# Optimization experiments

Measured on AMD Instinct MI355X. Metric: run time of the kernel, lower is better.

## Reference

```python
import jax, jax.numpy as jnp
import numpy as np

B = 1_000_000          # query points
D = 3                  # n_input_dims
N_LEVELS = 16
MIN_RES, MAX_RES = 16, 512
N_ENC = 2 ** 19        # max hashmap entries per level
N_EMBED = 2
INIT_SCALE = 1e-4
PRIMES = (1, 2654435761, 805459861)  # instant-ngp spatial-hash primes


def _resolutions():
    # Eq. 2/3 of instant-ngp: geometric growth from MIN_RES to MAX_RES
    growth = np.exp((np.log(MAX_RES) - np.log(MIN_RES)) / (N_LEVELS - 1))
    return [int(np.floor(MIN_RES * growth ** l)) for l in range(N_LEVELS)]

RES = _resolutions()
LEVEL_N_ENC = [min(r ** D, N_ENC) for r in RES]
LEVEL_HASH = [r ** D > N_ENC for r in RES]          # hash iff grid overflows table
CORNERS = np.stack(np.meshgrid(*([np.arange(2)] * D), indexing='ij'), -1).reshape(-1, D)  # (8,3)


def setup_inputs() -> dict:
    key = jax.random.key(0)
    ks = jax.random.split(key, N_LEVELS + 1)
    inp = {"x": jax.random.uniform(ks[0], (B, D), minval=-1.0, maxval=1.0, dtype=jnp.float32)}
    for l in range(N_LEVELS):
        inp[f"emb{l}"] = jax.random.uniform(
            ks[l + 1], (LEVEL_N_ENC[l], N_EMBED), minval=-INIT_SCALE, maxval=INIT_SCALE, dtype=jnp.float32
        )
    return inp


def _level_features(x, emb, res, n_enc, use_hash):
    # x: (B,3) in [-1,1] -> pixel coords, align_corners=False convention
    xp = (x + 1.0) * (res * 0.5) - 0.5
    x0 = jnp.floor(xp)
    t = xp - x0                                           # (B,3) fractional part
    ci = jnp.asarray(CORNERS, jnp.int32)                  # (8,3) corner offsets
    c = x0.astype(jnp.int32)[:, None, :] + ci[None]       # (B,8,3) corner coords
    off = jnp.asarray(CORNERS, xp.dtype)
    # trilinear weights: prod over dims of t or (1-t)
    w = jnp.prod(jnp.where(off[None] > 0, t[:, None, :], 1.0 - t[:, None, :]), axis=-1)  # (B,8)
    m = jnp.all((c >= 0) & (c < res), axis=-1)            # (B,8) zeros-padding mask
    if use_hash:
        cu = c.astype(jnp.uint32)
        h = cu[..., 0] * jnp.uint32(PRIMES[0])
        for d in range(1, D):
            h = h ^ (cu[..., d] * jnp.uint32(PRIMES[d]))
        ids = (h % jnp.uint32(n_enc)).astype(jnp.int32)
    else:
        # ravel index, x varies fastest ('xy' grid indexing)
        ids = (c[..., 0] + c[..., 1] * res + c[..., 2] * res * res) % n_enc
    ids = jnp.where(m, ids, 0)
    w = jnp.where(m, w, jnp.zeros_like(w))
    return jnp.sum(emb[ids] * w[..., None], axis=1)       # (B,E)


def reference(x, emb0, emb1, emb2, emb3, emb4, emb5, emb6, emb7,
              emb8, emb9, emb10, emb11, emb12, emb13, emb14, emb15):
    embs = [emb0, emb1, emb2, emb3, emb4, emb5, emb6, emb7,
            emb8, emb9, emb10, emb11, emb12, emb13, emb14, emb15]
    feats = [_level_features(x, embs[l], RES[l], LEVEL_N_ENC[l], LEVEL_HASH[l])
             for l in range(N_LEVELS)]
    return jnp.stack(feats, axis=1)  # (B, L, E)
```

## Files before the change

### kernel.cpp

```cpp
#include <hip/hip_runtime.h>
#include <stdint.h>


struct EmbPtrs { const float2* p[16]; };

constexpr int BLOCK = 256;
constexpr int kRes[16] = {16,20,25,32,40,50,64,80,101,128,161,203,256,322,406,512};

template<int RES_, bool HASH_>
__device__ __forceinline__ float2 level_feat(const float2* __restrict__ tab,
                                             float px, float py, float pz)
{
    constexpr uint32_t P1 = 2654435761u, P2 = 805459861u;
    constexpr uint32_t HMASK = (1u << 19) - 1u;

    const float rh = (float)RES_ * 0.5f;
    const float xp = (px + 1.0f) * rh - 0.5f;
    const float yp = (py + 1.0f) * rh - 0.5f;
    const float zp = (pz + 1.0f) * rh - 0.5f;
    const float fx = floorf(xp), fy = floorf(yp), fz = floorf(zp);
    const int ix = (int)fx, iy = (int)fy, iz = (int)fz;
    const float tx = xp - fx, ty = yp - fy, tz = zp - fz;

    const float wx[2] = {1.0f - tx, tx};
    const float wy[2] = {1.0f - ty, ty};
    const float wz[2] = {1.0f - tz, tz};
    const bool vx[2] = {(ix   >= 0) && (ix   < RES_), (ix+1 >= 0) && (ix+1 < RES_)};
    const bool vy[2] = {(iy   >= 0) && (iy   < RES_), (iy+1 >= 0) && (iy+1 < RES_)};
    const bool vz[2] = {(iz   >= 0) && (iz   < RES_), (iz+1 >= 0) && (iz+1 < RES_)};

    float ax = 0.0f, ay = 0.0f;

    if constexpr (!HASH_) {
        constexpr int r2 = RES_ * RES_;
        const int base = ix + iy * RES_ + iz * r2;
#pragma unroll
        for (int k = 0; k < 2; ++k)
#pragma unroll
        for (int j = 0; j < 2; ++j)
#pragma unroll
        for (int i = 0; i < 2; ++i) {
            const bool v = vx[i] && vy[j] && vz[k];
            const uint32_t idx = v ? (uint32_t)(base + i + j*RES_ + k*r2) : 0u;
            const float w = v ? (wx[i]*wy[j]*wz[k]) : 0.0f;
            const float2 e = tab[idx];
            ax = fmaf(e.x, w, ax);
            ay = fmaf(e.y, w, ay);
        }
    } else {
        const uint32_t hx0 = (uint32_t)ix;
        const uint32_t hy0 = (uint32_t)iy * P1;
        const uint32_t hz0 = (uint32_t)iz * P2;
        const uint32_t hx[2] = {hx0, hx0 + 1u};
        const uint32_t hy[2] = {hy0, hy0 + P1};
        const uint32_t hz[2] = {hz0, hz0 + P2};
#pragma unroll
        for (int k = 0; k < 2; ++k)
#pragma unroll
        for (int j = 0; j < 2; ++j)
#pragma unroll
        for (int i = 0; i < 2; ++i) {
            const bool v = vx[i] && vy[j] && vz[k];
            uint32_t idx = (hx[i] ^ hy[j] ^ hz[k]) & HMASK;
            idx = v ? idx : 0u;
            const float w = v ? (wx[i]*wy[j]*wz[k]) : 0.0f;
            const float2 e = tab[idx];
            ax = fmaf(e.x, w, ax);
            ay = fmaf(e.y, w, ay);
        }
    }
    return make_float2(ax, ay);
}

__global__ __launch_bounds__(BLOCK) void dense_kernel(
    const float* __restrict__ x, EmbPtrs embs, float4* __restrict__ out, int n)
{
    const int b = blockIdx.x * BLOCK + threadIdx.x;
    if (b >= n) return;
    const float px = x[3*b+0], py = x[3*b+1], pz = x[3*b+2];

    float2 f[8];
    f[0] = level_feat<16,false>(embs.p[0], px, py, pz);
    f[1] = level_feat<20,false>(embs.p[1], px, py, pz);
    f[2] = level_feat<25,false>(embs.p[2], px, py, pz);
    f[3] = level_feat<32,false>(embs.p[3], px, py, pz);
    f[4] = level_feat<40,false>(embs.p[4], px, py, pz);
    f[5] = level_feat<50,false>(embs.p[5], px, py, pz);
    f[6] = level_feat<64,false>(embs.p[6], px, py, pz);
    f[7] = level_feat<80,false>(embs.p[7], px, py, pz);

    float4* o = out + (size_t)b * 8;
#pragma unroll
    for (int i = 0; i < 4; ++i)
        o[i] = make_float4(f[2*i].x, f[2*i].y, f[2*i+1].x, f[2*i+1].y);
}

template<int L>
__global__ __launch_bounds__(BLOCK) void hash_level_kernel(
    const float* __restrict__ x, const float2* __restrict__ tab,
    float2* __restrict__ ws, int n)
{
    const int b = blockIdx.x * BLOCK + threadIdx.x;
    if (b >= n) return;
    const float px = x[3*b+0], py = x[3*b+1], pz = x[3*b+2];
    ws[b] = level_feat<kRes[L], true>(tab, px, py, pz);
}

__global__ __launch_bounds__(BLOCK) void merge_kernel(
    const float2* __restrict__ ws, float4* __restrict__ out, int n)
{
    const int b = blockIdx.x * BLOCK + threadIdx.x;
    if (b >= n) return;
    float2 f[8];
#pragma unroll
    for (int l = 0; l < 8; ++l)
        f[l] = ws[(size_t)l * n + b];
    float4* o = out + (size_t)b * 8 + 4;
#pragma unroll
    for (int i = 0; i < 4; ++i)
        o[i] = make_float4(f[2*i].x, f[2*i].y, f[2*i+1].x, f[2*i+1].y);
}

__global__ __launch_bounds__(BLOCK) void fallback_kernel(
    const float* __restrict__ x, EmbPtrs embs, float4* __restrict__ out, int n)
{
    const int b = blockIdx.x * BLOCK + threadIdx.x;
    if (b >= n) return;
    const float px = x[3*b+0], py = x[3*b+1], pz = x[3*b+2];
    float2 f[16];
    f[0]  = level_feat<16, false>(embs.p[0],  px, py, pz);
    f[1]  = level_feat<20, false>(embs.p[1],  px, py, pz);
    f[2]  = level_feat<25, false>(embs.p[2],  px, py, pz);
    f[3]  = level_feat<32, false>(embs.p[3],  px, py, pz);
    f[4]  = level_feat<40, false>(embs.p[4],  px, py, pz);
    f[5]  = level_feat<50, false>(embs.p[5],  px, py, pz);
    f[6]  = level_feat<64, false>(embs.p[6],  px, py, pz);
    f[7]  = level_feat<80, false>(embs.p[7],  px, py, pz);
    f[8]  = level_feat<101,true >(embs.p[8],  px, py, pz);
    f[9]  = level_feat<128,true >(embs.p[9],  px, py, pz);
    f[10] = level_feat<161,true >(embs.p[10], px, py, pz);
    f[11] = level_feat<203,true >(embs.p[11], px, py, pz);
    f[12] = level_feat<256,true >(embs.p[12], px, py, pz);
    f[13] = level_feat<322,true >(embs.p[13], px, py, pz);
    f[14] = level_feat<406,true >(embs.p[14], px, py, pz);
    f[15] = level_feat<512,true >(embs.p[15], px, py, pz);
    float4* o = out + (size_t)b * 8;
#pragma unroll
    for (int i = 0; i < 8; ++i)
        o[i] = make_float4(f[2*i].x, f[2*i].y, f[2*i+1].x, f[2*i+1].y);
}

extern "C" void kernel_launch(void* const* d_in, const int* in_sizes, int n_in,
                              void* d_out, int out_size, void* d_ws, size_t ws_size,
                              hipStream_t stream) {
    const float* x = (const float*)d_in[0];
    EmbPtrs embs;
    for (int l = 0; l < 16; ++l) embs.p[l] = (const float2*)d_in[1 + l];
    const int n = in_sizes[0] / 3;
    const int grid = (n + BLOCK - 1) / BLOCK;
    float4* out = (float4*)d_out;

    const size_t need = (size_t)8 * (size_t)n * sizeof(float2);
    if (ws_size >= need) {
        float2* ws = (float2*)d_ws;
        dense_kernel<<<grid, BLOCK, 0, stream>>>(x, embs, out, n);
        hash_level_kernel< 8><<<grid, BLOCK, 0, stream>>>(x, embs.p[ 8], ws + 0*(size_t)n, n);
        hash_level_kernel< 9><<<grid, BLOCK, 0, stream>>>(x, embs.p[ 9], ws + 1*(size_t)n, n);
        hash_level_kernel<10><<<grid, BLOCK, 0, stream>>>(x, embs.p[10], ws + 2*(size_t)n, n);
        hash_level_kernel<11><<<grid, BLOCK, 0, stream>>>(x, embs.p[11], ws + 3*(size_t)n, n);
        hash_level_kernel<12><<<grid, BLOCK, 0, stream>>>(x, embs.p[12], ws + 4*(size_t)n, n);
        hash_level_kernel<13><<<grid, BLOCK, 0, stream>>>(x, embs.p[13], ws + 5*(size_t)n, n);
        hash_level_kernel<14><<<grid, BLOCK, 0, stream>>>(x, embs.p[14], ws + 6*(size_t)n, n);
        hash_level_kernel<15><<<grid, BLOCK, 0, stream>>>(x, embs.p[15], ws + 7*(size_t)n, n);
        merge_kernel<<<grid, BLOCK, 0, stream>>>(ws, out, n);
    } else {
        fallback_kernel<<<grid, BLOCK, 0, stream>>>(x, embs, out, n);
    }
}
```

Measured before the change: 681.6 us.

## Pair x-adjacent corner gathers into float4 loads and vectorize hash-level merge

Trilinear corner gathers are restructured so the two x-neighbouring corners share one 16-byte load. In the dense levels this applies when both corners are valid and the index is even. In the hash levels it applies when the x coordinate is even: the x prime is 1, so the two hashes differ only in bit 0. Each hash-level thread now processes two points, and when n is even the merge kernel reads float4 pairs from the workspace. The aim is fewer gather instructions and more memory-level parallelism, at the cost of extra branches, select logic and register pressure.

```diff
diff --git a/kernel.cpp b/kernel.cpp
--- a/kernel.cpp
+++ b/kernel.cpp
@@ -6,67 +6,101 @@
 
 constexpr int BLOCK = 256;
 constexpr int kRes[16] = {16,20,25,32,40,50,64,80,101,128,161,203,256,322,406,512};
-
-template<int RES_, bool HASH_>
-__device__ __forceinline__ float2 level_feat(const float2* __restrict__ tab,
-                                             float px, float py, float pz)
-{
-    constexpr uint32_t P1 = 2654435761u, P2 = 805459861u;
-    constexpr uint32_t HMASK = (1u << 19) - 1u;
-
+constexpr uint32_t P1 = 2654435761u, P2 = 805459861u;
+constexpr uint32_t HMASK = (1u << 19) - 1u;
+
+struct Tri {
+    int ix, iy, iz;
+    float wx[2], wy[2], wz[2];
+    bool vx[2], vy[2], vz[2];
+};
+
+template<int RES_>
+__device__ __forceinline__ Tri tri_setup(float px, float py, float pz)
+{
+    Tri s;
     const float rh = (float)RES_ * 0.5f;
     const float xp = (px + 1.0f) * rh - 0.5f;
     const float yp = (py + 1.0f) * rh - 0.5f;
     const float zp = (pz + 1.0f) * rh - 0.5f;
     const float fx = floorf(xp), fy = floorf(yp), fz = floorf(zp);
-    const int ix = (int)fx, iy = (int)fy, iz = (int)fz;
+    s.ix = (int)fx; s.iy = (int)fy; s.iz = (int)fz;
     const float tx = xp - fx, ty = yp - fy, tz = zp - fz;
-
-    const float wx[2] = {1.0f - tx, tx};
-    const float wy[2] = {1.0f - ty, ty};
-    const float wz[2] = {1.0f - tz, tz};
-    const bool vx[2] = {(ix   >= 0) && (ix   < RES_), (ix+1 >= 0) && (ix+1 < RES_)};
-    const bool vy[2] = {(iy   >= 0) && (iy   < RES_), (iy+1 >= 0) && (iy+1 < RES_)};
-    const bool vz[2] = {(iz   >= 0) && (iz   < RES_), (iz+1 >= 0) && (iz+1 < RES_)};
-
+    s.wx[0] = 1.0f - tx; s.wx[1] = tx;
+    s.wy[0] = 1.0f - ty; s.wy[1] = ty;
+    s.wz[0] = 1.0f - tz; s.wz[1] = tz;
+    s.vx[0] = (s.ix   >= 0) && (s.ix   < RES_); s.vx[1] = (s.ix+1 >= 0) && (s.ix+1 < RES_);
+    s.vy[0] = (s.iy   >= 0) && (s.iy   < RES_); s.vy[1] = (s.iy+1 >= 0) && (s.iy+1 < RES_);
+    s.vz[0] = (s.iz   >= 0) && (s.iz   < RES_); s.vz[1] = (s.iz+1 >= 0) && (s.iz+1 < RES_);
+    return s;
+}
+
+template<int RES_>
+__device__ __forceinline__ float2 dense_feat(const float2* __restrict__ tab,
+                                             float px, float py, float pz)
+{
+    const Tri s = tri_setup<RES_>(px, py, pz);
+    constexpr int r2 = RES_ * RES_;
+    const int base = s.ix + s.iy * RES_ + s.iz * r2;
     float ax = 0.0f, ay = 0.0f;
-
-    if constexpr (!HASH_) {
-        constexpr int r2 = RES_ * RES_;
-        const int base = ix + iy * RES_ + iz * r2;
-#pragma unroll
-        for (int k = 0; k < 2; ++k)
-#pragma unroll
-        for (int j = 0; j < 2; ++j)
-#pragma unroll
-        for (int i = 0; i < 2; ++i) {
-            const bool v = vx[i] && vy[j] && vz[k];
-            const uint32_t idx = v ? (uint32_t)(base + i + j*RES_ + k*r2) : 0u;
-            const float w = v ? (wx[i]*wy[j]*wz[k]) : 0.0f;
-            const float2 e = tab[idx];
-            ax = fmaf(e.x, w, ax);
-            ay = fmaf(e.y, w, ay);
+#pragma unroll
+    for (int k = 0; k < 2; ++k)
+#pragma unroll
+    for (int j = 0; j < 2; ++j) {
+        const bool vyz = s.vy[j] && s.vz[k];
+        const float wyz = s.wy[j] * s.wz[k];
+        const int i0 = base + j * RES_ + k * r2;
+        const float w0 = (vyz && s.vx[0]) ? s.wx[0] * wyz : 0.0f;
+        const float w1 = (vyz && s.vx[1]) ? s.wx[1] * wyz : 0.0f;
+        if (vyz && s.vx[0] && s.vx[1] && !(i0 & 1)) {
+            const float4 q = *(const float4*)(tab + i0);
+            ax = fmaf(q.x, w0, ax); ay = fmaf(q.y, w0, ay);
+            ax = fmaf(q.z, w1, ax); ay = fmaf(q.w, w1, ay);
+        } else {
+            const uint32_t a0 = (vyz && s.vx[0]) ? (uint32_t)i0       : 0u;
+            const uint32_t a1 = (vyz && s.vx[1]) ? (uint32_t)(i0 + 1) : 0u;
+            const float2 e0 = tab[a0];
+            const float2 e1 = tab[a1];
+            ax = fmaf(e0.x, w0, ax); ay = fmaf(e0.y, w0, ay);
+            ax = fmaf(e1.x, w1, ax); ay = fmaf(e1.y, w1, ay);
         }
-    } else {
-        const uint32_t hx0 = (uint32_t)ix;
-        const uint32_t hy0 = (uint32_t)iy * P1;
-        const uint32_t hz0 = (uint32_t)iz * P2;
-        const uint32_t hx[2] = {hx0, hx0 + 1u};
-        const uint32_t hy[2] = {hy0, hy0 + P1};
-        const uint32_t hz[2] = {hz0, hz0 + P2};
-#pragma unroll
-        for (int k = 0; k < 2; ++k)
-#pragma unroll
-        for (int j = 0; j < 2; ++j)
-#pragma unroll
-        for (int i = 0; i < 2; ++i) {
-            const bool v = vx[i] && vy[j] && vz[k];
-            uint32_t idx = (hx[i] ^ hy[j] ^ hz[k]) & HMASK;
-            idx = v ? idx : 0u;
-            const float w = v ? (wx[i]*wy[j]*wz[k]) : 0.0f;
-            const float2 e = tab[idx];
-            ax = fmaf(e.x, w, ax);
-            ay = fmaf(e.y, w, ay);
+    }
+    return make_float2(ax, ay);
+}
+
+template<int RES_>
+__device__ __forceinline__ float2 hash_feat(const float2* __restrict__ tab,
+                                            float px, float py, float pz)
+{
+    const Tri s = tri_setup<RES_>(px, py, pz);
+    const uint32_t hy0 = (uint32_t)s.iy * P1;
+    const uint32_t hz0 = (uint32_t)s.iz * P2;
+    const uint32_t hy[2] = {hy0, hy0 + P1};
+    const uint32_t hz[2] = {hz0, hz0 + P2};
+    const uint32_t ux = (uint32_t)s.ix;
+    float ax = 0.0f, ay = 0.0f;
+#pragma unroll
+    for (int k = 0; k < 2; ++k)
+#pragma unroll
+    for (int j = 0; j < 2; ++j) {
+        const bool vyz = s.vy[j] && s.vz[k];
+        const float wyz = s.wy[j] * s.wz[k];
+        const uint32_t E = hy[j] ^ hz[k];
+        const uint32_t J0 = (ux ^ E) & HMASK;
+        const uint32_t J1 = ((ux + 1u) ^ E) & HMASK;
+        const float w0 = (vyz && s.vx[0]) ? s.wx[0] * wyz : 0.0f;
+        const float w1 = (vyz && s.vx[1]) ? s.wx[1] * wyz : 0.0f;
+        if (!(ux & 1u)) {
+            const float4 q = *(const float4*)(tab + (J0 & ~1u));
+            const float wl = (J0 & 1u) ? w1 : w0;
+            const float wh = (J0 & 1u) ? w0 : w1;
+            ax = fmaf(q.x, wl, ax); ay = fmaf(q.y, wl, ay);
+            ax = fmaf(q.z, wh, ax); ay = fmaf(q.w, wh, ay);
+        } else {
+            const float2 e0 = tab[J0];
+            const float2 e1 = tab[J1];
+            ax = fmaf(e0.x, w0, ax); ay = fmaf(e0.y, w0, ay);
+            ax = fmaf(e1.x, w1, ax); ay = fmaf(e1.y, w1, ay);
         }
     }
     return make_float2(ax, ay);
@@ -80,14 +114,14 @@
     const float px = x[3*b+0], py = x[3*b+1], pz = x[3*b+2];
 
     float2 f[8];
-    f[0] = level_feat<16,false>(embs.p[0], px, py, pz);
-    f[1] = level_feat<20,false>(embs.p[1], px, py, pz);
-    f[2] = level_feat<25,false>(embs.p[2], px, py, pz);
-    f[3] = level_feat<32,false>(embs.p[3], px, py, pz);
-    f[4] = level_feat<40,false>(embs.p[4], px, py, pz);
-    f[5] = level_feat<50,false>(embs.p[5], px, py, pz);
-    f[6] = level_feat<64,false>(embs.p[6], px, py, pz);
-    f[7] = level_feat<80,false>(embs.p[7], px, py, pz);
+    f[0] = dense_feat<16>(embs.p[0], px, py, pz);
+    f[1] = dense_feat<20>(embs.p[1], px, py, pz);
+    f[2] = dense_feat<25>(embs.p[2], px, py, pz);
+    f[3] = dense_feat<32>(embs.p[3], px, py, pz);
+    f[4] = dense_feat<40>(embs.p[4], px, py, pz);
+    f[5] = dense_feat<50>(embs.p[5], px, py, pz);
+    f[6] = dense_feat<64>(embs.p[6], px, py, pz);
+    f[7] = dense_feat<80>(embs.p[7], px, py, pz);
 
     float4* o = out + (size_t)b * 8;
 #pragma unroll
@@ -100,13 +134,35 @@
     const float* __restrict__ x, const float2* __restrict__ tab,
     float2* __restrict__ ws, int n)
 {
-    const int b = blockIdx.x * BLOCK + threadIdx.x;
-    if (b >= n) return;
-    const float px = x[3*b+0], py = x[3*b+1], pz = x[3*b+2];
-    ws[b] = level_feat<kRes[L], true>(tab, px, py, pz);
-}
-
-__global__ __launch_bounds__(BLOCK) void merge_kernel(
+    const int h = (n + 1) >> 1;
+    const int b = blockIdx.x * BLOCK + threadIdx.x;
+    if (b >= h) return;
+    ws[b] = hash_feat<kRes[L]>(tab, x[3*b+0], x[3*b+1], x[3*b+2]);
+    const int p1 = b + h;
+    if (p1 < n)
+        ws[p1] = hash_feat<kRes[L]>(tab, x[3*p1+0], x[3*p1+1], x[3*p1+2]);
+}
+
+__global__ __launch_bounds__(BLOCK) void merge_kernel2(
+    const float2* __restrict__ ws, float4* __restrict__ out, int n)
+{
+    const int t = blockIdx.x * BLOCK + threadIdx.x;
+    if (t >= (n >> 1)) return;
+    const int p0 = 2 * t;
+    float4 q[8];
+#pragma unroll
+    for (int l = 0; l < 8; ++l)
+        q[l] = *(const float4*)(ws + (size_t)l * n + p0);
+    float4* o0 = out + (size_t)p0 * 8 + 4;
+    float4* o1 = out + (size_t)(p0 + 1) * 8 + 4;
+#pragma unroll
+    for (int i = 0; i < 4; ++i) {
+        o0[i] = make_float4(q[2*i].x, q[2*i].y, q[2*i+1].x, q[2*i+1].y);
+        o1[i] = make_float4(q[2*i].z, q[2*i].w, q[2*i+1].z, q[2*i+1].w);
+    }
+}
+
+__global__ __launch_bounds__(BLOCK) void merge_kernel1(
     const float2* __restrict__ ws, float4* __restrict__ out, int n)
 {
     const int b = blockIdx.x * BLOCK + threadIdx.x;
@@ -128,22 +184,22 @@
     if (b >= n) return;
     const float px = x[3*b+0], py = x[3*b+1], pz = x[3*b+2];
     float2 f[16];
-    f[0]  = level_feat<16, false>(embs.p[0],  px, py, pz);
-    f[1]  = level_feat<20, false>(embs.p[1],  px, py, pz);
-    f[2]  = level_feat<25, false>(embs.p[2],  px, py, pz);
-    f[3]  = level_feat<32, false>(embs.p[3],  px, py, pz);
-    f[4]  = level_feat<40, false>(embs.p[4],  px, py, pz);
-    f[5]  = level_feat<50, false>(embs.p[5],  px, py, pz);
-    f[6]  = level_feat<64, false>(embs.p[6],  px, py, pz);
-    f[7]  = level_feat<80, false>(embs.p[7],  px, py, pz);
-    f[8]  = level_feat<101,true >(embs.p[8],  px, py, pz);
-    f[9]  = level_feat<128,true >(embs.p[9],  px, py, pz);
-    f[10] = level_feat<161,true >(embs.p[10], px, py, pz);
-    f[11] = level_feat<203,true >(embs.p[11], px, py, pz);
-    f[12] = level_feat<256,true >(embs.p[12], px, py, pz);
-    f[13] = level_feat<322,true >(embs.p[13], px, py, pz);
-    f[14] = level_feat<406,true >(embs.p[14], px, py, pz);
-    f[15] = level_feat<512,true >(embs.p[15], px, py, pz);
+    f[0]  = dense_feat<16 >(embs.p[0],  px, py, pz);
+    f[1]  = dense_feat<20 >(embs.p[1],  px, py, pz);
+    f[2]  = dense_feat<25 >(embs.p[2],  px, py, pz);
+    f[3]  = dense_feat<32 >(embs.p[3],  px, py, pz);
+    f[4]  = dense_feat<40 >(embs.p[4],  px, py, pz);
+    f[5]  = dense_feat<50 >(embs.p[5],  px, py, pz);
+    f[6]  = dense_feat<64 >(embs.p[6],  px, py, pz);
+    f[7]  = dense_feat<80 >(embs.p[7],  px, py, pz);
+    f[8]  = hash_feat<101>(embs.p[8],  px, py, pz);
+    f[9]  = hash_feat<128>(embs.p[9],  px, py, pz);
+    f[10] = hash_feat<161>(embs.p[10], px, py, pz);
+    f[11] = hash_feat<203>(embs.p[11], px, py, pz);
+    f[12] = hash_feat<256>(embs.p[12], px, py, pz);
+    f[13] = hash_feat<322>(embs.p[13], px, py, pz);
+    f[14] = hash_feat<406>(embs.p[14], px, py, pz);
+    f[15] = hash_feat<512>(embs.p[15], px, py, pz);
     float4* o = out + (size_t)b * 8;
 #pragma unroll
     for (int i = 0; i < 8; ++i)
@@ -157,22 +213,26 @@
     EmbPtrs embs;
     for (int l = 0; l < 16; ++l) embs.p[l] = (const float2*)d_in[1 + l];
     const int n = in_sizes[0] / 3;
-    const int grid = (n + BLOCK - 1) / BLOCK;
+    const int grid  = (n + BLOCK - 1) / BLOCK;
+    const int hgrid = (((n + 1) >> 1) + BLOCK - 1) / BLOCK;
     float4* out = (float4*)d_out;
 
     const size_t need = (size_t)8 * (size_t)n * sizeof(float2);
     if (ws_size >= need) {
         float2* ws = (float2*)d_ws;
         dense_kernel<<<grid, BLOCK, 0, stream>>>(x, embs, out, n);
-        hash_level_kernel< 8><<<grid, BLOCK, 0, stream>>>(x, embs.p[ 8], ws + 0*(size_t)n, n);
-        hash_level_kernel< 9><<<grid, BLOCK, 0, stream>>>(x, embs.p[ 9], ws + 1*(size_t)n, n);
-        hash_level_kernel<10><<<grid, BLOCK, 0, stream>>>(x, embs.p[10], ws + 2*(size_t)n, n);
-        hash_level_kernel<11><<<grid, BLOCK, 0, stream>>>(x, embs.p[11], ws + 3*(size_t)n, n);
-        hash_level_kernel<12><<<grid, BLOCK, 0, stream>>>(x, embs.p[12], ws + 4*(size_t)n, n);
-        hash_level_kernel<13><<<grid, BLOCK, 0, stream>>>(x, embs.p[13], ws + 5*(size_t)n, n);
-        hash_level_kernel<14><<<grid, BLOCK, 0, stream>>>(x, embs.p[14], ws + 6*(size_t)n, n);
-        hash_level_kernel<15><<<grid, BLOCK, 0, stream>>>(x, embs.p[15], ws + 7*(size_t)n, n);
-        merge_kernel<<<grid, BLOCK, 0, stream>>>(ws, out, n);
+        hash_level_kernel< 8><<<hgrid, BLOCK, 0, stream>>>(x, embs.p[ 8], ws + 0*(size_t)n, n);
+        hash_level_kernel< 9><<<hgrid, BLOCK, 0, stream>>>(x, embs.p[ 9], ws + 1*(size_t)n, n);
+        hash_level_kernel<10><<<hgrid, BLOCK, 0, stream>>>(x, embs.p[10], ws + 2*(size_t)n, n);
+        hash_level_kernel<11><<<hgrid, BLOCK, 0, stream>>>(x, embs.p[11], ws + 3*(size_t)n, n);
+        hash_level_kernel<12><<<hgrid, BLOCK, 0, stream>>>(x, embs.p[12], ws + 4*(size_t)n, n);
+        hash_level_kernel<13><<<hgrid, BLOCK, 0, stream>>>(x, embs.p[13], ws + 5*(size_t)n, n);
+        hash_level_kernel<14><<<hgrid, BLOCK, 0, stream>>>(x, embs.p[14], ws + 6*(size_t)n, n);
+        hash_level_kernel<15><<<hgrid, BLOCK, 0, stream>>>(x, embs.p[15], ws + 7*(size_t)n, n);
+        if ((n & 1) == 0)
+            merge_kernel2<<<hgrid, BLOCK, 0, stream>>>(ws, out, n);
+        else
+            merge_kernel1<<<grid, BLOCK, 0, stream>>>(ws, out, n);
     } else {
         fallback_kernel<<<grid, BLOCK, 0, stream>>>(x, embs, out, n);
     }
```

Measured after the change: 708.5 us. +3.9%, slower.
